# Kernel optimization log

Hardware: AMD Instinct MI355X
Metric: run time of the kernel (lower is better)

Reference implementation:

```python
import jax, jax.numpy as jnp
import numpy as np

B, S, D = 2, 2048, 4096
H, KV, HD = 32, 8, 128
THETA = 10000.0


def rotate_half(x):
    x1, x2 = x[..., : HD // 2], x[..., HD // 2 :]
    return jnp.concatenate((-x2, x1), axis=-1)


def setup_inputs() -> dict:
    key = jax.random.key(0)
    ks = jax.random.split(key, 8)
    s = 1.0 / np.sqrt(D)
    return {
        "hidden_states": jax.random.normal(ks[0], (B, S, D), jnp.float32),
        "modality_indicators": jax.random.randint(ks[1], (B, S), 0, 2, jnp.int64 if jax.config.jax_enable_x64 else jnp.int32),
        "position_ids": jnp.arange(S, dtype=jnp.int32),
        "Wq": jax.random.normal(ks[2], (D, H * HD), jnp.float32) * s,
        "Wk0": jax.random.normal(ks[3], (D, KV * HD), jnp.float32) * s,
        "Wk1": jax.random.normal(ks[4], (D, KV * HD), jnp.float32) * s,
        "Wv0": jax.random.normal(ks[5], (D, KV * HD), jnp.float32) * s,
        "Wv1": jax.random.normal(ks[6], (D, KV * HD), jnp.float32) * s,
        "Wo": jax.random.normal(ks[7], (H * HD, D), jnp.float32) * s,
    }


def reference(hidden_states, modality_indicators, position_ids, Wq, Wk0, Wk1, Wv0, Wv1, Wo):
    x = hidden_states
    # Multiway (modality-routed) k/v projections: per-token select between two linears.
    sel = (modality_indicators == 1)[..., None]  # [B,S,1]
    q = x @ Wq                                   # [B,S,H*HD]
    k = jnp.where(sel, x @ Wk1, x @ Wk0)         # [B,S,KV*HD]
    v = jnp.where(sel, x @ Wv1, x @ Wv0)

    q = q.reshape(B, S, H, HD).transpose(0, 2, 1, 3)    # [B,H,S,HD]
    k = k.reshape(B, S, KV, HD).transpose(0, 2, 1, 3)   # [B,KV,S,HD]
    v = v.reshape(B, S, KV, HD).transpose(0, 2, 1, 3)

    # RoPE cache and application (emb = cat(freqs, freqs))
    inv_freq = 1.0 / (THETA ** (jnp.arange(0, HD, 2, dtype=jnp.float32) / HD))
    freqs = position_ids.astype(jnp.float32)[:, None] * inv_freq[None, :]   # [S,HD/2]
    emb = jnp.concatenate((freqs, freqs), axis=-1)                          # [S,HD]
    cos = jnp.cos(emb)[None, None, :, :]                                    # [1,1,S,HD]
    sin = jnp.sin(emb)[None, None, :, :]
    q = q * cos + rotate_half(q) * sin
    k = k * cos + rotate_half(k) * sin

    # GQA: repeat kv heads
    n_rep = H // KV
    k = jnp.repeat(k, n_rep, axis=1)  # [B,H,S,HD]
    v = jnp.repeat(v, n_rep, axis=1)

    scores = jnp.einsum("bhqd,bhkd->bhqk", q, k) / np.sqrt(HD)
    causal = jnp.tril(jnp.ones((S, S), dtype=bool))
    scores = jnp.where(causal[None, None], scores, jnp.finfo(scores.dtype).min)
    attn = jax.nn.softmax(scores, axis=-1)
    ctx = jnp.einsum("bhqk,bhkd->bhqd", attn, v)            # [B,H,S,HD]
    ctx = ctx.transpose(0, 2, 1, 3).reshape(B, S, H * HD)
    return ctx @ Wo
```

## Files before the change

kernel.cpp:

```cpp
#include <hip/hip_runtime.h>

typedef unsigned short u16;
typedef unsigned int   u32;
using bf16x8 = __attribute__((ext_vector_type(8))) __bf16;
using f32x4  = __attribute__((ext_vector_type(4))) float;
using f32x16 = __attribute__((ext_vector_type(16))) float;
using u32x4  = __attribute__((ext_vector_type(4))) unsigned int;
using ushort8 = __attribute__((ext_vector_type(8))) unsigned short;


__device__ __forceinline__ u16 f2bf(float f) {
  u32 u = __builtin_bit_cast(u32, f);
  return (u16)((u + 0x7fffu + ((u >> 16) & 1u)) >> 16);
}
__device__ __forceinline__ float bf2f(u16 h) {
  return __builtin_bit_cast(float, (u32)h << 16);
}
__device__ __forceinline__ f32x4 mfma16(bf16x8 a, bf16x8 b, f32x4 c) {
  return __builtin_amdgcn_mfma_f32_16x16x32_bf16(a, b, c, 0, 0, 0);
}
__device__ __forceinline__ f32x16 mfma32(bf16x8 a, bf16x8 b, f32x16 c) {
  return __builtin_amdgcn_mfma_f32_32x32x16_bf16(a, b, c, 0, 0, 0);
}
__device__ __forceinline__ f32x16 zero16() {
  f32x16 z;
#pragma unroll
  for (int i = 0; i < 16; ++i) z[i] = 0.f;
  return z;
}
__device__ __forceinline__ void g2l16(const void* gp, void* lp) {
  __builtin_amdgcn_global_load_lds(
      (__attribute__((address_space(1))) void*)(void*)gp,
      (__attribute__((address_space(3))) void*)lp, 16, 0, 0);
}

__global__ void k_cvt(const float* __restrict__ in, u16* __restrict__ out, int n4) {
  int i = blockIdx.x * 256 + threadIdx.x;
  if (i >= n4) return;
  float4 v = ((const float4*)in)[i];
  ushort4 o;
  o.x = f2bf(v.x); o.y = f2bf(v.y); o.z = f2bf(v.z); o.w = f2bf(v.w);
  ((ushort4*)out)[i] = o;
}

__global__ __launch_bounds__(256) void k_tcvt(const float* __restrict__ in, u16* __restrict__ out,
                                              int K, int N) {
  __shared__ u16 t[64][72];
  const int n0 = blockIdx.x * 64, k0 = blockIdx.y * 64;
  const int tid = threadIdx.x;
  const int r = tid >> 2, c4 = (tid & 3) * 16;
  const float* src = in + (size_t)(k0 + r) * N + n0 + c4;
#pragma unroll
  for (int q = 0; q < 4; ++q) {
    float4 v = *(const float4*)(src + 4 * q);
    t[c4 + 4 * q + 0][r] = f2bf(v.x);
    t[c4 + 4 * q + 1][r] = f2bf(v.y);
    t[c4 + 4 * q + 2][r] = f2bf(v.z);
    t[c4 + 4 * q + 3][r] = f2bf(v.w);
  }
  __syncthreads();
  u16* dst = out + (size_t)(n0 + r) * K + k0 + c4;
#pragma unroll
  for (int hh = 0; hh < 2; ++hh)
    *(ushort8*)(dst + 8 * hh) = *(const ushort8*)(&t[r][c4 + 8 * hh]);
}

__global__ void k_scan(const int* __restrict__ mod, int* __restrict__ perm, int* __restrict__ meta) {
  __shared__ int ps[1024];
  const int b = blockIdx.x, t = threadIdx.x;
  perm[b * 2304 + t] = -1;
  perm[b * 2304 + 1024 + t] = -1;
  if (t < 256) perm[b * 2304 + 2048 + t] = -1;
  const int i0 = 2 * t, i1 = 2 * t + 1;
  const int f0 = (mod[b * 2048 + i0] != 1) ? 1 : 0;
  const int f1 = (mod[b * 2048 + i1] != 1) ? 1 : 0;
  const int sum = f0 + f1;
  ps[t] = sum;
  __syncthreads();
  for (int off = 1; off < 1024; off <<= 1) {
    int v = (t >= off) ? ps[t - off] : 0;
    __syncthreads();
    ps[t] += v;
    __syncthreads();
  }
  const int total0 = ps[1023];
  const int excl = ps[t] - sum;
  const int nt0 = (total0 + 255) >> 8;
  const int off1 = nt0 * 256;
  const int s0 = f0 ? excl : off1 + (i0 - excl);
  const int s1 = f1 ? (excl + f0) : off1 + (i1 - (excl + f0));
  perm[b * 2304 + s0] = i0;
  perm[b * 2304 + s1] = i1;
  if (t == 0) { meta[b * 2] = total0; meta[b * 2 + 1] = nt0; }
}

#define TILE_BODY(T, VMLIT, DOSTAGE)                                         \
  {                                                                          \
    asm volatile("s_waitcnt vmcnt(" VMLIT ")" ::: "memory");                 \
    __builtin_amdgcn_s_barrier();                                            \
    __builtin_amdgcn_sched_barrier(0);                                       \
    const u16* base_ = lds + ((T) & 3) * 16384;                              \
    bf16x8 bfr[4], afr[4];                                                   \
    _Pragma("unroll")                                                        \
    for (int nf = 0; nf < 4; ++nf)                                           \
      bfr[nf] = *(const bf16x8*)(base_ + boff + nf * 512);                   \
    _Pragma("unroll")                                                        \
    for (int mf = 0; mf < 4; ++mf)                                           \
      afr[mf] = *(const bf16x8*)(base_ + aoff + mf * 512);                   \
    if (DOSTAGE) stageA((T) + 3);                                            \
    asm volatile("s_waitcnt lgkmcnt(0)" ::: "memory");                       \
    __builtin_amdgcn_sched_barrier(0);                                       \
    __builtin_amdgcn_s_setprio(1);                                           \
    _Pragma("unroll")                                                        \
    for (int mf = 0; mf < 4; ++mf)                                           \
      _Pragma("unroll")                                                      \
      for (int nf = 0; nf < 4; ++nf)                                         \
        acc[mf][nf] = mfma16(afr[mf], bfr[nf], acc[mf][nf]);                 \
    __builtin_amdgcn_s_setprio(0);                                           \
    __builtin_amdgcn_s_barrier();                                            \
    _Pragma("unroll")                                                        \
    for (int mf = 0; mf < 4; ++mf)                                           \
      afr[mf] = *(const bf16x8*)(base_ + aoff + (mf + 4) * 512);             \
    if (DOSTAGE) stageB((T) + 3);                                            \
    asm volatile("s_waitcnt lgkmcnt(0)" ::: "memory");                       \
    __builtin_amdgcn_sched_barrier(0);                                       \
    __builtin_amdgcn_s_setprio(1);                                           \
    _Pragma("unroll")                                                        \
    for (int mf = 0; mf < 4; ++mf)                                           \
      _Pragma("unroll")                                                      \
      for (int nf = 0; nf < 4; ++nf)                                         \
        acc[mf + 4][nf] = mfma16(afr[mf], bfr[nf], acc[mf + 4][nf]);         \
    __builtin_amdgcn_s_setprio(0);                                           \
  }

#define GEMM_MAIN_LOOP()                                                     \
  stageA(0); stageB(0); stageA(1); stageB(1); stageA(2); stageB(2);          \
  for (int t = 0; t < 125; ++t) TILE_BODY(t, "8", true);                     \
  TILE_BODY(125, "8", false);                                                \
  TILE_BODY(126, "4", false);                                                \
  TILE_BODY(127, "0", false);

__global__ __launch_bounds__(512, 2) void k_gemm8(const u16* __restrict__ A, const u16* __restrict__ Bt,
                                                  float* __restrict__ Cp) {
  __shared__ u16 lds[4 * 16384];
  const int tid = threadIdx.x, wid = tid >> 6, l = tid & 63, g = l >> 4, li = l & 15;
  const int wr = wid >> 2, wc = wid & 3;
  const int bid = blockIdx.x;
  const int swz = (bid & 7) * 32 + (bid >> 3);
  const int m0 = (swz >> 4) * 256, n0 = (swz & 15) * 256;

  const int bo = wid * 2048 + l * 16;
  const int srow = bo >> 6;
  const int sgg = (l & 3) ^ ((l >> 3) & 3);
  const u16* pA0 = A + (size_t)(m0 + srow) * 4096 + sgg * 8;
  const u16* pA1 = pA0 + (size_t)16 * 4096;
  const u16* pB0 = Bt + (size_t)(n0 + srow) * 4096 + sgg * 8;
  const u16* pB1 = pB0 + (size_t)16 * 4096;

  auto stageA = [&](int t) {
    u16* da = (u16*)lds + (t & 3) * 16384 + wid * 1024;
    g2l16(pA0 + t * 32, da);
    g2l16(pA1 + t * 32, da + 512);
  };
  auto stageB = [&](int t) {
    u16* db = (u16*)lds + (t & 3) * 16384 + wid * 1024 + 8192;
    g2l16(pB0 + t * 32, db);
    g2l16(pB1 + t * 32, db + 512);
  };

  const int lsl8 = (g ^ ((li >> 1) & 3)) * 8;
  const int aoff = (wr * 128 + li) * 32 + lsl8;
  const int boff = 8192 + (wc * 64 + li) * 32 + lsl8;

  const f32x4 vzero = {0.f, 0.f, 0.f, 0.f};
  f32x4 acc[8][4];
#pragma unroll
  for (int m = 0; m < 8; ++m)
#pragma unroll
    for (int n = 0; n < 4; ++n) acc[m][n] = vzero;

  GEMM_MAIN_LOOP();

#pragma unroll
  for (int mf = 0; mf < 8; ++mf)
#pragma unroll
    for (int nf = 0; nf < 4; ++nf)
#pragma unroll
      for (int j = 0; j < 4; ++j) {
        int row = m0 + wr * 128 + mf * 16 + g * 4 + j;
        int col = n0 + wc * 64 + nf * 16 + li;
        Cp[(size_t)row * 4096 + col] = acc[mf][nf][j];
      }
}

__global__ __launch_bounds__(512, 2) void k_gemmQKV(const u16* __restrict__ Xb, const u16* __restrict__ WqT,
                                                    const u16* __restrict__ B0, const u16* __restrict__ B1,
                                                    const int* __restrict__ perm, const int* __restrict__ meta,
                                                    u16* __restrict__ Qr, u16* __restrict__ Ksel,
                                                    u16* __restrict__ Vsel) {
  __shared__ u16 lds[4 * 16384];
  const int tid = threadIdx.x, wid = tid >> 6, l = tid & 63, g = l >> 4, li = l & 15;
  const int wr = wid >> 2, wc = wid & 3;
  const int bid = blockIdx.x;
  const bool isQ = bid < 256;

  const int bo = wid * 2048 + l * 16;
  const int srow = bo >> 6;
  const int sgg = (l & 3) ^ ((l >> 3) & 3);

  int m0 = 0, n0 = 0, bb = 0, tm = 0;
  const u16 *pA0, *pA1, *pB0;
  if (isQ) {
    const int swz = (bid & 7) * 32 + (bid >> 3);
    m0 = (swz >> 4) * 256; n0 = (swz & 15) * 256;
    pA0 = Xb + (size_t)(m0 + srow) * 4096 + sgg * 8;
    pA1 = pA0 + (size_t)16 * 4096;
    pB0 = WqT + (size_t)(n0 + srow) * 4096 + sgg * 8;
  } else {
    const int kb = bid - 256;
    const int seg = kb >> 3;
    n0 = (kb & 7) * 256;
    bb = seg / 9; tm = seg % 9;
    const int nt0 = meta[bb * 2 + 1];
    const u16* Bt = (tm >= nt0) ? B1 : B0;
    int t0 = perm[bb * 2304 + tm * 256 + srow];
    int t1 = perm[bb * 2304 + tm * 256 + srow + 16];
    if (t0 < 0) t0 = 0;
    if (t1 < 0) t1 = 0;
    pA0 = Xb + ((size_t)bb * 2048 + t0) * 4096 + sgg * 8;
    pA1 = Xb + ((size_t)bb * 2048 + t1) * 4096 + sgg * 8;
    pB0 = Bt + (size_t)(n0 + srow) * 4096 + sgg * 8;
  }
  const u16* pB1 = pB0 + (size_t)16 * 4096;

  auto stageA = [&](int t) {
    u16* da = (u16*)lds + (t & 3) * 16384 + wid * 1024;
    g2l16(pA0 + t * 32, da);
    g2l16(pA1 + t * 32, da + 512);
  };
  auto stageB = [&](int t) {
    u16* db = (u16*)lds + (t & 3) * 16384 + wid * 1024 + 8192;
    g2l16(pB0 + t * 32, db);
    g2l16(pB1 + t * 32, db + 512);
  };

  const int lsl8 = (g ^ ((li >> 1) & 3)) * 8;
  const int aoff = (wr * 128 + li) * 32 + lsl8;
  const int boff = 8192 + (wc * 64 + li) * 32 + lsl8;

  const f32x4 vzero = {0.f, 0.f, 0.f, 0.f};
  f32x4 acc[8][4];
#pragma unroll
  for (int m = 0; m < 8; ++m)
#pragma unroll
    for (int n = 0; n < 4; ++n) acc[m][n] = vzero;

  GEMM_MAIN_LOOP();

  if (isQ) {
#pragma unroll
    for (int mf = 0; mf < 8; ++mf)
#pragma unroll
      for (int nf = 0; nf < 4; ++nf)
#pragma unroll
        for (int j = 0; j < 4; ++j) {
          int row = m0 + wr * 128 + mf * 16 + g * 4 + j;
          int col = n0 + wc * 64 + nf * 16 + li;
          int b = row >> 11, s = row & 2047, h = col >> 7, d = col & 127;
          Qr[(((size_t)(b * 32 + h)) * 2048 + s) * 128 + d] = f2bf(acc[mf][nf][j]);
        }
  } else {
#pragma unroll
    for (int mf = 0; mf < 8; ++mf)
#pragma unroll
      for (int nf = 0; nf < 4; ++nf)
#pragma unroll
        for (int j = 0; j < 4; ++j) {
          int slot = tm * 256 + wr * 128 + mf * 16 + g * 4 + j;
          int tok = perm[bb * 2304 + slot];
          if (tok >= 0) {
            int col = n0 + wc * 64 + nf * 16 + li;
            int kv = col >> 10, hh = (col >> 7) & 7, d = col & 127;
            u16* dst = (kv ? Vsel : Ksel) + (((size_t)(bb * 8 + hh)) * 2048 + tok) * 128 + d;
            *dst = f2bf(acc[mf][nf][j]);
          }
        }
  }
}

__global__ void k_ropeq(u16* __restrict__ Q, const int* __restrict__ pos) {
  int row = blockIdx.x * 4 + (threadIdx.x >> 6);
  int l = threadIdx.x & 63;
  int s = row & 2047;
  u16* p = Q + (size_t)row * 128;
  float x1 = bf2f(p[l]), x2 = bf2f(p[l + 64]);
  float ang = (float)pos[s] * expf((float)l * -0.14391156831212787f);
  float cs = cosf(ang), sn = sinf(ang);
  const float sc = 0.08838834764831845f;
  p[l] = f2bf((x1 * cs - x2 * sn) * sc);
  p[l + 64] = f2bf((x2 * cs + x1 * sn) * sc);
}

__global__ void k_kvprep(const u16* __restrict__ Ks, const u16* __restrict__ Vs,
                         const int* __restrict__ pos,
                         u16* __restrict__ Kr, u16* __restrict__ Vt) {
  __shared__ u16 Vl[64][136];
  int blk = blockIdx.x;
  int st = blk & 31, kvh = (blk >> 5) & 7, b = blk >> 8;
  int s0 = st * 64;
  int tid = threadIdx.x, wid = tid >> 6, l = tid & 63;
  float invf = expf((float)l * -0.14391156831212787f);
  size_t slab = (size_t)(b * 8 + kvh) * 2048;
  for (int rr = 0; rr < 16; ++rr) {
    int r = wid * 16 + rr;
    int s = s0 + r;
    const u16* ks = Ks + (slab + s) * 128;
    const u16* vs = Vs + (slab + s) * 128;
    float ang = (float)pos[s] * invf;
    float cs = cosf(ang), sn = sinf(ang);
    float x1 = bf2f(ks[l]), x2 = bf2f(ks[l + 64]);
    u16* kd = Kr + (slab + s) * 128;
    kd[l] = f2bf(x1 * cs - x2 * sn);
    kd[l + 64] = f2bf(x2 * cs + x1 * sn);
    Vl[r][l] = vs[l];
    Vl[r][l + 64] = vs[l + 64];
  }
  __syncthreads();
  int d = tid >> 1, si0 = (tid & 1) * 32;
  u16* vd = Vt + ((size_t)(b * 8 + kvh) * 128 + d) * 2048 + s0 + si0;
#pragma unroll
  for (int k4 = 0; k4 < 8; ++k4) {
    ushort4 o;
    o.x = Vl[si0 + k4 * 4 + 0][d];
    o.y = Vl[si0 + k4 * 4 + 1][d];
    o.z = Vl[si0 + k4 * 4 + 2][d];
    o.w = Vl[si0 + k4 * 4 + 3][d];
    *(ushort4*)(vd + k4 * 4) = o;
  }
}

__global__ __launch_bounds__(256, 2) void k_attn(const u16* __restrict__ Q, const u16* __restrict__ Kr,
                                                 const u16* __restrict__ Vt, u16* __restrict__ ctx) {
  __shared__ u16 Kl[2 * 64 * 128];
  __shared__ u16 Vl[2 * 128 * 64];
  const int bh = blockIdx.x;
  const int p = blockIdx.y;
  const int b = bh >> 5, h = bh & 31, kvh = h >> 2;
  const int tid = threadIdx.x, w = tid >> 6, l = tid & 63;
  const int lo5 = l & 31, hi = l >> 5;
  const bool hib = hi != 0;
  const size_t kvslab = (size_t)(b * 8 + kvh) * 2048;
  const u16* Kg = Kr + kvslab * 128;
  const u16* Vg = Vt + kvslab * 128;
  const float L2E = 1.4426950408889634f;

  auto stage = [&](int kt, int bi) {
#pragma unroll
    for (int i = 0; i < 4; ++i) {
      int c = w * 4 + i;
      int slot = c * 1024 + l * 16;
      {
        int row = slot >> 8;
        int inner = (slot & 255) ^ ((row & 15) << 4);
        g2l16((const char*)Kg + kt * 16384 + row * 256 + inner,
              (char*)Kl + bi * 16384 + c * 1024);
      }
      {
        int row = slot >> 7;
        int inner = (slot & 127) ^ ((row & 7) << 4);
        g2l16((const char*)Vg + (size_t)row * 4096 + kt * 128 + inner,
              (char*)Vl + bi * 16384 + c * 1024);
      }
    }
  };

  for (int hf = 0; hf < 2; ++hf) {
    const int qi = hf ? (15 - p) : p;
    const int q0 = qi * 128;
    const int qlane = q0 + w * 32 + lo5;
    const u16* qrow = Q + ((size_t)bh * 2048 + qlane) * 128;
    bf16x8 qf[8];
#pragma unroll
    for (int kk = 0; kk < 8; ++kk) qf[kk] = *(const bf16x8*)(qrow + kk * 16 + hi * 8);

    f32x16 ot[4];
#pragma unroll
    for (int i = 0; i < 4; ++i) ot[i] = zero16();
    float m = -1e30f, ls = 0.f;

    const int nkt = 2 * qi + 2;
    stage(0, 0);
    stage(1, 1);
    for (int kt = 0; kt < nkt; ++kt) {
      if (kt + 1 < nkt) {
        asm volatile("s_waitcnt vmcnt(8)" ::: "memory");
      } else {
        asm volatile("s_waitcnt vmcnt(0)" ::: "memory");
      }
      __builtin_amdgcn_s_barrier();
      __builtin_amdgcn_sched_barrier(0);
      const char* kbase = (const char*)Kl + (kt & 1) * 16384;
      const char* vbase = (const char*)Vl + (kt & 1) * 16384;
      const int ktb = kt * 64;
      if (ktb <= q0 + w * 32 + 31) {
        f32x16 st[2];
        st[0] = zero16(); st[1] = zero16();
#pragma unroll
        for (int kk = 0; kk < 8; ++kk) {
          bf16x8 kfr[2];
#pragma unroll
          for (int mf = 0; mf < 2; ++mf) {
            int row = mf * 32 + lo5;
            kfr[mf] = *(const bf16x8*)(kbase + row * 256 + ((kk * 32 + hi * 16) ^ ((row & 15) << 4)));
          }
          __builtin_amdgcn_s_setprio(1);
          st[0] = mfma32(kfr[0], qf[kk], st[0]);
          st[1] = mfma32(kfr[1], qf[kk], st[1]);
          __builtin_amdgcn_s_setprio(0);
        }
        if (ktb + 63 > q0 + w * 32) {
#pragma unroll
          for (int mf = 0; mf < 2; ++mf)
#pragma unroll
            for (int r = 0; r < 16; ++r) {
              int kg = ktb + mf * 32 + (r & 3) + 8 * (r >> 2) + 4 * hi;
              if (kg > qlane) st[mf][r] = -3.0e38f;
            }
        }
        float t[16];
#pragma unroll
        for (int r = 0; r < 16; ++r) t[r] = fmaxf(st[0][r], st[1][r]);
#pragma unroll
        for (int s = 8; s >= 1; s >>= 1)
#pragma unroll
          for (int r = 0; r < s; ++r) t[r] = fmaxf(t[r], t[r + s]);
        float pmax = fmaxf(t[0], __shfl_xor(t[0], 32));
        if (!__all(pmax <= m + 8.f)) {
          float nm = fmaxf(m, pmax);
          float resc = exp2f((m - nm) * L2E);
          m = nm;
          ls *= resc;
#pragma unroll
          for (int i = 0; i < 4; ++i)
#pragma unroll
            for (int r = 0; r < 16; ++r) ot[i][r] *= resc;
        }
#pragma unroll
        for (int mf = 0; mf < 2; ++mf)
#pragma unroll
          for (int r = 0; r < 16; ++r) st[mf][r] = exp2f((st[mf][r] - m) * L2E);
        float u[16];
#pragma unroll
        for (int r = 0; r < 16; ++r) u[r] = st[0][r] + st[1][r];
#pragma unroll
        for (int s = 8; s >= 1; s >>= 1)
#pragma unroll
          for (int r = 0; r < s; ++r) u[r] += u[r + s];
        ls += u[0] + __shfl_xor(u[0], 32);
        u32 pkv[16];
#pragma unroll
        for (int mf = 0; mf < 2; ++mf)
#pragma unroll
          for (int tt = 0; tt < 8; ++tt) {
            u32 r;
            asm("v_cvt_pk_bf16_f32 %0, %1, %2" : "=v"(r) : "v"(st[mf][2 * tt]), "v"(st[mf][2 * tt + 1]));
            pkv[mf * 8 + tt] = r;
          }
        bf16x8 pfrag[4];
#pragma unroll
        for (int kk = 0; kk < 4; ++kk) {
          int c = (kk >> 1) * 8 + (kk & 1) * 4;
          u32 m0 = hib ? pkv[c + 2] : pkv[c + 0];
          u32 m1 = hib ? pkv[c + 3] : pkv[c + 1];
          u32 s0 = hib ? pkv[c + 0] : pkv[c + 2];
          u32 s1 = hib ? pkv[c + 1] : pkv[c + 3];
          u32 r0 = (u32)__shfl_xor((int)s0, 32);
          u32 r1 = (u32)__shfl_xor((int)s1, 32);
          u32x4 wv = {hib ? r0 : m0, hib ? r1 : m1, hib ? m0 : r0, hib ? m1 : r1};
          pfrag[kk] = __builtin_bit_cast(bf16x8, wv);
        }
#pragma unroll
        for (int mfV = 0; mfV < 4; ++mfV) {
          int row = mfV * 32 + lo5;
          const char* vb = vbase + row * 128;
          int sw = (row & 7) << 4;
          bf16x8 vf[4];
#pragma unroll
          for (int kk = 0; kk < 4; ++kk)
            vf[kk] = *(const bf16x8*)(vb + ((kk * 32 + hi * 16) ^ sw));
          __builtin_amdgcn_s_setprio(1);
#pragma unroll
          for (int kk = 0; kk < 4; ++kk) ot[mfV] = mfma32(vf[kk], pfrag[kk], ot[mfV]);
          __builtin_amdgcn_s_setprio(0);
        }
      }
      __builtin_amdgcn_s_barrier();
      if (kt + 2 < nkt) stage(kt + 2, kt & 1);
    }
    float inv = 1.0f / ls;
    u16* crow = ctx + ((size_t)(b * 2048) + qlane) * 4096 + h * 128;
#pragma unroll
    for (int mfV = 0; mfV < 4; ++mfV)
#pragma unroll
      for (int rq = 0; rq < 4; ++rq) {
        ushort4 o4;
        o4.x = f2bf(ot[mfV][rq * 4 + 0] * inv);
        o4.y = f2bf(ot[mfV][rq * 4 + 1] * inv);
        o4.z = f2bf(ot[mfV][rq * 4 + 2] * inv);
        o4.w = f2bf(ot[mfV][rq * 4 + 3] * inv);
        *(ushort4*)(crow + mfV * 32 + rq * 8 + hi * 4) = o4;
      }
  }
}

extern "C" void kernel_launch(void* const* d_in, const int* in_sizes, int n_in,
                              void* d_out, int out_size, void* d_ws, size_t ws_size,
                              hipStream_t stream) {
  (void)in_sizes; (void)n_in; (void)out_size; (void)ws_size;
  const float* X   = (const float*)d_in[0];
  const int*   mod = (const int*)d_in[1];
  const int*   pos = (const int*)d_in[2];
  const float* Wq  = (const float*)d_in[3];
  const float* Wk0 = (const float*)d_in[4];
  const float* Wk1 = (const float*)d_in[5];
  const float* Wv0 = (const float*)d_in[6];
  const float* Wv1 = (const float*)d_in[7];
  const float* Wo  = (const float*)d_in[8];
  float* out = (float*)d_out;

  u16* p = (u16*)d_ws;
  auto take = [&](size_t n) { u16* r = p; p += n; return r; };
  u16* Xb    = take(16777216);
  u16* WqT   = take(16777216);
  u16* WoT   = take(16777216);
  u16* Wkv0T = take(8388608);
  u16* Wkv1T = take(8388608);
  u16* Qr    = take(16777216);
  u16* Ksel  = take(4194304);
  u16* Vsel  = take(4194304);
  int* perm  = (int*)take(9216);
  int* meta  = (int*)take(64);
  u16* Kr  = WqT;
  u16* Vtr = WqT + 4194304;
  u16* ctx = Xb;

  k_cvt<<<dim3(16384), 256, 0, stream>>>(X, Xb, 4194304);
  k_scan<<<dim3(2), 1024, 0, stream>>>(mod, perm, meta);
  k_tcvt<<<dim3(64, 64), 256, 0, stream>>>(Wq, WqT, 4096, 4096);
  k_tcvt<<<dim3(16, 64), 256, 0, stream>>>(Wk0, Wkv0T,                4096, 1024);
  k_tcvt<<<dim3(16, 64), 256, 0, stream>>>(Wv0, Wkv0T + 1024 * 4096,  4096, 1024);
  k_tcvt<<<dim3(16, 64), 256, 0, stream>>>(Wk1, Wkv1T,                4096, 1024);
  k_tcvt<<<dim3(16, 64), 256, 0, stream>>>(Wv1, Wkv1T + 1024 * 4096,  4096, 1024);
  k_tcvt<<<dim3(64, 64), 256, 0, stream>>>(Wo, WoT, 4096, 4096);

  k_gemmQKV<<<dim3(400), 512, 0, stream>>>(Xb, WqT, Wkv0T, Wkv1T, perm, meta, Qr, Ksel, Vsel);

  k_ropeq<<<dim3(32768), 256, 0, stream>>>(Qr, pos);
  k_kvprep<<<dim3(512), 256, 0, stream>>>(Ksel, Vsel, pos, Kr, Vtr);

  k_attn<<<dim3(64, 8), 256, 0, stream>>>(Qr, Kr, Vtr, ctx);

  k_gemm8<<<dim3(256), 512, 0, stream>>>(ctx, WoT, out);
}
```

Baseline: 566.2 us.

## Use 16-wave GEMM blocks with single-barrier tiles and fuse prep kernel launches

Both GEMM kernels move from 512 to 1024 threads. Each wave now computes a 64x64 sub-tile instead of 128x64, stages one A and one B chunk per tile, and each K-step has one barrier instead of two, with the manual LDS waits dropped. Separately, the four K/V weight transposes are merged with the Wq transpose into one launch, and the Q RoPE and K/V RoPE-plus-V-transpose kernels are merged into one launch. The Wo transpose is moved after attention. The intent is to raise MFMA occupancy and latency hiding and to cut launch overhead. The risks are extra register pressure from the (1024,4) launch bound, which asks for more resident waves than a CU supports, and looser scheduling control without the sched barriers.

```diff
diff --git a/kernel.cpp b/kernel.cpp
--- a/kernel.cpp
+++ b/kernel.cpp
@@ -43,10 +43,9 @@
   ((ushort4*)out)[i] = o;
 }
 
-__global__ __launch_bounds__(256) void k_tcvt(const float* __restrict__ in, u16* __restrict__ out,
-                                              int K, int N) {
-  __shared__ u16 t[64][72];
-  const int n0 = blockIdx.x * 64, k0 = blockIdx.y * 64;
+__device__ __forceinline__ void tcvt_tile(const float* __restrict__ in, u16* __restrict__ out,
+                                          int K, int N, int nt, int kt, u16 (*t)[72]) {
+  const int n0 = nt * 64, k0 = kt * 64;
   const int tid = threadIdx.x;
   const int r = tid >> 2, c4 = (tid & 3) * 16;
   const float* src = in + (size_t)(k0 + r) * N + n0 + c4;
@@ -63,6 +62,30 @@
 #pragma unroll
   for (int hh = 0; hh < 2; ++hh)
     *(ushort8*)(dst + 8 * hh) = *(const ushort8*)(&t[r][c4 + 8 * hh]);
+}
+
+__global__ __launch_bounds__(256) void k_tcvt(const float* __restrict__ in, u16* __restrict__ out,
+                                              int K, int N) {
+  __shared__ u16 t[64][72];
+  tcvt_tile(in, out, K, N, blockIdx.x, blockIdx.y, t);
+}
+
+__global__ __launch_bounds__(256) void k_tcvt5(const float* __restrict__ Wq, const float* __restrict__ Wk0,
+                                               const float* __restrict__ Wv0, const float* __restrict__ Wk1,
+                                               const float* __restrict__ Wv1, u16* __restrict__ WqT,
+                                               u16* __restrict__ Wkv0T, u16* __restrict__ Wkv1T) {
+  __shared__ u16 t[64][72];
+  int bid = blockIdx.x;
+  if (bid < 4096) {
+    tcvt_tile(Wq, WqT, 4096, 4096, bid & 63, bid >> 6, t);
+  } else {
+    int r = bid - 4096;
+    int mat = r >> 10, rr = r & 1023;
+    const float* src = (mat == 0) ? Wk0 : (mat == 1) ? Wv0 : (mat == 2) ? Wk1 : Wv1;
+    u16* dst = (mat == 0) ? Wkv0T : (mat == 1) ? (Wkv0T + (size_t)1024 * 4096)
+                                  : (mat == 2) ? Wkv1T : (Wkv1T + (size_t)1024 * 4096);
+    tcvt_tile(src, dst, 4096, 1024, rr & 15, rr >> 4, t);
+  }
 }
 
 __global__ void k_scan(const int* __restrict__ mod, int* __restrict__ perm, int* __restrict__ meta) {
@@ -107,9 +130,7 @@
     _Pragma("unroll")                                                        \
     for (int mf = 0; mf < 4; ++mf)                                           \
       afr[mf] = *(const bf16x8*)(base_ + aoff + mf * 512);                   \
-    if (DOSTAGE) stageA((T) + 3);                                            \
-    asm volatile("s_waitcnt lgkmcnt(0)" ::: "memory");                       \
-    __builtin_amdgcn_sched_barrier(0);                                       \
+    if (DOSTAGE) stage((T) + 3);                                             \
     __builtin_amdgcn_s_setprio(1);                                           \
     _Pragma("unroll")                                                        \
     for (int mf = 0; mf < 4; ++mf)                                           \
@@ -117,31 +138,17 @@
       for (int nf = 0; nf < 4; ++nf)                                         \
         acc[mf][nf] = mfma16(afr[mf], bfr[nf], acc[mf][nf]);                 \
     __builtin_amdgcn_s_setprio(0);                                           \
-    __builtin_amdgcn_s_barrier();                                            \
-    _Pragma("unroll")                                                        \
-    for (int mf = 0; mf < 4; ++mf)                                           \
-      afr[mf] = *(const bf16x8*)(base_ + aoff + (mf + 4) * 512);             \
-    if (DOSTAGE) stageB((T) + 3);                                            \
-    asm volatile("s_waitcnt lgkmcnt(0)" ::: "memory");                       \
-    __builtin_amdgcn_sched_barrier(0);                                       \
-    __builtin_amdgcn_s_setprio(1);                                           \
-    _Pragma("unroll")                                                        \
-    for (int mf = 0; mf < 4; ++mf)                                           \
-      _Pragma("unroll")                                                      \
-      for (int nf = 0; nf < 4; ++nf)                                         \
-        acc[mf + 4][nf] = mfma16(afr[mf], bfr[nf], acc[mf + 4][nf]);         \
-    __builtin_amdgcn_s_setprio(0);                                           \
   }
 
 #define GEMM_MAIN_LOOP()                                                     \
-  stageA(0); stageB(0); stageA(1); stageB(1); stageA(2); stageB(2);          \
-  for (int t = 0; t < 125; ++t) TILE_BODY(t, "8", true);                     \
-  TILE_BODY(125, "8", false);                                                \
-  TILE_BODY(126, "4", false);                                                \
+  stage(0); stage(1); stage(2);                                              \
+  for (int t = 0; t < 125; ++t) TILE_BODY(t, "4", true);                     \
+  TILE_BODY(125, "4", false);                                                \
+  TILE_BODY(126, "2", false);                                                \
   TILE_BODY(127, "0", false);
 
-__global__ __launch_bounds__(512, 2) void k_gemm8(const u16* __restrict__ A, const u16* __restrict__ Bt,
-                                                  float* __restrict__ Cp) {
+__global__ __launch_bounds__(1024, 4) void k_gemm8(const u16* __restrict__ A, const u16* __restrict__ Bt,
+                                                   float* __restrict__ Cp) {
   __shared__ u16 lds[4 * 16384];
   const int tid = threadIdx.x, wid = tid >> 6, l = tid & 63, g = l >> 4, li = l & 15;
   const int wr = wid >> 2, wc = wid & 3;
@@ -149,73 +156,63 @@
   const int swz = (bid & 7) * 32 + (bid >> 3);
   const int m0 = (swz >> 4) * 256, n0 = (swz & 15) * 256;
 
-  const int bo = wid * 2048 + l * 16;
-  const int srow = bo >> 6;
+  const int srow = wid * 16 + (l >> 2);
   const int sgg = (l & 3) ^ ((l >> 3) & 3);
-  const u16* pA0 = A + (size_t)(m0 + srow) * 4096 + sgg * 8;
-  const u16* pA1 = pA0 + (size_t)16 * 4096;
-  const u16* pB0 = Bt + (size_t)(n0 + srow) * 4096 + sgg * 8;
-  const u16* pB1 = pB0 + (size_t)16 * 4096;
-
-  auto stageA = [&](int t) {
-    u16* da = (u16*)lds + (t & 3) * 16384 + wid * 1024;
-    g2l16(pA0 + t * 32, da);
-    g2l16(pA1 + t * 32, da + 512);
+  const u16* pA = A + (size_t)(m0 + srow) * 4096 + sgg * 8;
+  const u16* pB = Bt + (size_t)(n0 + srow) * 4096 + sgg * 8;
+
+  auto stage = [&](int t) {
+    u16* da = (u16*)lds + (t & 3) * 16384 + wid * 512;
+    g2l16(pA + t * 32, da);
+    g2l16(pB + t * 32, da + 8192);
   };
-  auto stageB = [&](int t) {
-    u16* db = (u16*)lds + (t & 3) * 16384 + wid * 1024 + 8192;
-    g2l16(pB0 + t * 32, db);
-    g2l16(pB1 + t * 32, db + 512);
-  };
 
   const int lsl8 = (g ^ ((li >> 1) & 3)) * 8;
-  const int aoff = (wr * 128 + li) * 32 + lsl8;
+  const int aoff = (wr * 64 + li) * 32 + lsl8;
   const int boff = 8192 + (wc * 64 + li) * 32 + lsl8;
 
   const f32x4 vzero = {0.f, 0.f, 0.f, 0.f};
-  f32x4 acc[8][4];
-#pragma unroll
-  for (int m = 0; m < 8; ++m)
+  f32x4 acc[4][4];
+#pragma unroll
+  for (int m = 0; m < 4; ++m)
 #pragma unroll
     for (int n = 0; n < 4; ++n) acc[m][n] = vzero;
 
   GEMM_MAIN_LOOP();
 
 #pragma unroll
-  for (int mf = 0; mf < 8; ++mf)
+  for (int mf = 0; mf < 4; ++mf)
 #pragma unroll
     for (int nf = 0; nf < 4; ++nf)
 #pragma unroll
       for (int j = 0; j < 4; ++j) {
-        int row = m0 + wr * 128 + mf * 16 + g * 4 + j;
+        int row = m0 + wr * 64 + mf * 16 + g * 4 + j;
         int col = n0 + wc * 64 + nf * 16 + li;
         Cp[(size_t)row * 4096 + col] = acc[mf][nf][j];
       }
 }
 
-__global__ __launch_bounds__(512, 2) void k_gemmQKV(const u16* __restrict__ Xb, const u16* __restrict__ WqT,
-                                                    const u16* __restrict__ B0, const u16* __restrict__ B1,
-                                                    const int* __restrict__ perm, const int* __restrict__ meta,
-                                                    u16* __restrict__ Qr, u16* __restrict__ Ksel,
-                                                    u16* __restrict__ Vsel) {
+__global__ __launch_bounds__(1024, 4) void k_gemmQKV(const u16* __restrict__ Xb, const u16* __restrict__ WqT,
+                                                     const u16* __restrict__ B0, const u16* __restrict__ B1,
+                                                     const int* __restrict__ perm, const int* __restrict__ meta,
+                                                     u16* __restrict__ Qr, u16* __restrict__ Ksel,
+                                                     u16* __restrict__ Vsel) {
   __shared__ u16 lds[4 * 16384];
   const int tid = threadIdx.x, wid = tid >> 6, l = tid & 63, g = l >> 4, li = l & 15;
   const int wr = wid >> 2, wc = wid & 3;
   const int bid = blockIdx.x;
   const bool isQ = bid < 256;
 
-  const int bo = wid * 2048 + l * 16;
-  const int srow = bo >> 6;
+  const int srow = wid * 16 + (l >> 2);
   const int sgg = (l & 3) ^ ((l >> 3) & 3);
 
   int m0 = 0, n0 = 0, bb = 0, tm = 0;
-  const u16 *pA0, *pA1, *pB0;
+  const u16 *pA, *pB;
   if (isQ) {
     const int swz = (bid & 7) * 32 + (bid >> 3);
     m0 = (swz >> 4) * 256; n0 = (swz & 15) * 256;
-    pA0 = Xb + (size_t)(m0 + srow) * 4096 + sgg * 8;
-    pA1 = pA0 + (size_t)16 * 4096;
-    pB0 = WqT + (size_t)(n0 + srow) * 4096 + sgg * 8;
+    pA = Xb + (size_t)(m0 + srow) * 4096 + sgg * 8;
+    pB = WqT + (size_t)(n0 + srow) * 4096 + sgg * 8;
   } else {
     const int kb = bid - 256;
     const int seg = kb >> 3;
@@ -224,34 +221,25 @@
     const int nt0 = meta[bb * 2 + 1];
     const u16* Bt = (tm >= nt0) ? B1 : B0;
     int t0 = perm[bb * 2304 + tm * 256 + srow];
-    int t1 = perm[bb * 2304 + tm * 256 + srow + 16];
     if (t0 < 0) t0 = 0;
-    if (t1 < 0) t1 = 0;
-    pA0 = Xb + ((size_t)bb * 2048 + t0) * 4096 + sgg * 8;
-    pA1 = Xb + ((size_t)bb * 2048 + t1) * 4096 + sgg * 8;
-    pB0 = Bt + (size_t)(n0 + srow) * 4096 + sgg * 8;
-  }
-  const u16* pB1 = pB0 + (size_t)16 * 4096;
-
-  auto stageA = [&](int t) {
-    u16* da = (u16*)lds + (t & 3) * 16384 + wid * 1024;
-    g2l16(pA0 + t * 32, da);
-    g2l16(pA1 + t * 32, da + 512);
+    pA = Xb + ((size_t)bb * 2048 + t0) * 4096 + sgg * 8;
+    pB = Bt + (size_t)(n0 + srow) * 4096 + sgg * 8;
+  }
+
+  auto stage = [&](int t) {
+    u16* da = (u16*)lds + (t & 3) * 16384 + wid * 512;
+    g2l16(pA + t * 32, da);
+    g2l16(pB + t * 32, da + 8192);
   };
-  auto stageB = [&](int t) {
-    u16* db = (u16*)lds + (t & 3) * 16384 + wid * 1024 + 8192;
-    g2l16(pB0 + t * 32, db);
-    g2l16(pB1 + t * 32, db + 512);
-  };
 
   const int lsl8 = (g ^ ((li >> 1) & 3)) * 8;
-  const int aoff = (wr * 128 + li) * 32 + lsl8;
+  const int aoff = (wr * 64 + li) * 32 + lsl8;
   const int boff = 8192 + (wc * 64 + li) * 32 + lsl8;
 
   const f32x4 vzero = {0.f, 0.f, 0.f, 0.f};
-  f32x4 acc[8][4];
-#pragma unroll
-  for (int m = 0; m < 8; ++m)
+  f32x4 acc[4][4];
+#pragma unroll
+  for (int m = 0; m < 4; ++m)
 #pragma unroll
     for (int n = 0; n < 4; ++n) acc[m][n] = vzero;
 
@@ -259,24 +247,24 @@
 
   if (isQ) {
 #pragma unroll
-    for (int mf = 0; mf < 8; ++mf)
+    for (int mf = 0; mf < 4; ++mf)
 #pragma unroll
       for (int nf = 0; nf < 4; ++nf)
 #pragma unroll
         for (int j = 0; j < 4; ++j) {
-          int row = m0 + wr * 128 + mf * 16 + g * 4 + j;
+          int row = m0 + wr * 64 + mf * 16 + g * 4 + j;
           int col = n0 + wc * 64 + nf * 16 + li;
           int b = row >> 11, s = row & 2047, h = col >> 7, d = col & 127;
           Qr[(((size_t)(b * 32 + h)) * 2048 + s) * 128 + d] = f2bf(acc[mf][nf][j]);
         }
   } else {
 #pragma unroll
-    for (int mf = 0; mf < 8; ++mf)
+    for (int mf = 0; mf < 4; ++mf)
 #pragma unroll
       for (int nf = 0; nf < 4; ++nf)
 #pragma unroll
         for (int j = 0; j < 4; ++j) {
-          int slot = tm * 256 + wr * 128 + mf * 16 + g * 4 + j;
+          int slot = tm * 256 + wr * 64 + mf * 16 + g * 4 + j;
           int tok = perm[bb * 2304 + slot];
           if (tok >= 0) {
             int col = n0 + wc * 64 + nf * 16 + li;
@@ -288,54 +276,55 @@
   }
 }
 
-__global__ void k_ropeq(u16* __restrict__ Q, const int* __restrict__ pos) {
-  int row = blockIdx.x * 4 + (threadIdx.x >> 6);
-  int l = threadIdx.x & 63;
-  int s = row & 2047;
-  u16* p = Q + (size_t)row * 128;
-  float x1 = bf2f(p[l]), x2 = bf2f(p[l + 64]);
-  float ang = (float)pos[s] * expf((float)l * -0.14391156831212787f);
-  float cs = cosf(ang), sn = sinf(ang);
-  const float sc = 0.08838834764831845f;
-  p[l] = f2bf((x1 * cs - x2 * sn) * sc);
-  p[l + 64] = f2bf((x2 * cs + x1 * sn) * sc);
-}
-
-__global__ void k_kvprep(const u16* __restrict__ Ks, const u16* __restrict__ Vs,
-                         const int* __restrict__ pos,
-                         u16* __restrict__ Kr, u16* __restrict__ Vt) {
+__global__ __launch_bounds__(256) void k_ropekv(u16* __restrict__ Q, const u16* __restrict__ Ks,
+                                                const u16* __restrict__ Vs, const int* __restrict__ pos,
+                                                u16* __restrict__ Kr, u16* __restrict__ Vt) {
   __shared__ u16 Vl[64][136];
-  int blk = blockIdx.x;
-  int st = blk & 31, kvh = (blk >> 5) & 7, b = blk >> 8;
-  int s0 = st * 64;
-  int tid = threadIdx.x, wid = tid >> 6, l = tid & 63;
-  float invf = expf((float)l * -0.14391156831212787f);
-  size_t slab = (size_t)(b * 8 + kvh) * 2048;
-  for (int rr = 0; rr < 16; ++rr) {
-    int r = wid * 16 + rr;
-    int s = s0 + r;
-    const u16* ks = Ks + (slab + s) * 128;
-    const u16* vs = Vs + (slab + s) * 128;
+  const int bid = blockIdx.x;
+  const int tid = threadIdx.x, l = tid & 63;
+  const float invf = expf((float)l * -0.14391156831212787f);
+  if (bid < 32768) {
+    int row = bid * 4 + (tid >> 6);
+    int s = row & 2047;
+    u16* p = Q + (size_t)row * 128;
+    float x1 = bf2f(p[l]), x2 = bf2f(p[l + 64]);
     float ang = (float)pos[s] * invf;
     float cs = cosf(ang), sn = sinf(ang);
-    float x1 = bf2f(ks[l]), x2 = bf2f(ks[l + 64]);
-    u16* kd = Kr + (slab + s) * 128;
-    kd[l] = f2bf(x1 * cs - x2 * sn);
-    kd[l + 64] = f2bf(x2 * cs + x1 * sn);
-    Vl[r][l] = vs[l];
-    Vl[r][l + 64] = vs[l + 64];
-  }
-  __syncthreads();
-  int d = tid >> 1, si0 = (tid & 1) * 32;
-  u16* vd = Vt + ((size_t)(b * 8 + kvh) * 128 + d) * 2048 + s0 + si0;
-#pragma unroll
-  for (int k4 = 0; k4 < 8; ++k4) {
-    ushort4 o;
-    o.x = Vl[si0 + k4 * 4 + 0][d];
-    o.y = Vl[si0 + k4 * 4 + 1][d];
-    o.z = Vl[si0 + k4 * 4 + 2][d];
-    o.w = Vl[si0 + k4 * 4 + 3][d];
-    *(ushort4*)(vd + k4 * 4) = o;
+    const float sc = 0.08838834764831845f;
+    p[l] = f2bf((x1 * cs - x2 * sn) * sc);
+    p[l + 64] = f2bf((x2 * cs + x1 * sn) * sc);
+  } else {
+    int blk = bid - 32768;
+    int st = blk & 31, kvh = (blk >> 5) & 7, b = blk >> 8;
+    int s0 = st * 64;
+    int wid = tid >> 6;
+    size_t slab = (size_t)(b * 8 + kvh) * 2048;
+    for (int rr = 0; rr < 16; ++rr) {
+      int r = wid * 16 + rr;
+      int s = s0 + r;
+      const u16* ks = Ks + (slab + s) * 128;
+      const u16* vs = Vs + (slab + s) * 128;
+      float ang = (float)pos[s] * invf;
+      float cs = cosf(ang), sn = sinf(ang);
+      float x1 = bf2f(ks[l]), x2 = bf2f(ks[l + 64]);
+      u16* kd = Kr + (slab + s) * 128;
+      kd[l] = f2bf(x1 * cs - x2 * sn);
+      kd[l + 64] = f2bf(x2 * cs + x1 * sn);
+      Vl[r][l] = vs[l];
+      Vl[r][l + 64] = vs[l + 64];
+    }
+    __syncthreads();
+    int d = tid >> 1, si0 = (tid & 1) * 32;
+    u16* vd = Vt + ((size_t)(b * 8 + kvh) * 128 + d) * 2048 + s0 + si0;
+#pragma unroll
+    for (int k4 = 0; k4 < 8; ++k4) {
+      ushort4 o;
+      o.x = Vl[si0 + k4 * 4 + 0][d];
+      o.y = Vl[si0 + k4 * 4 + 1][d];
+      o.z = Vl[si0 + k4 * 4 + 2][d];
+      o.w = Vl[si0 + k4 * 4 + 3][d];
+      *(ushort4*)(vd + k4 * 4) = o;
+    }
   }
 }
 
@@ -546,19 +535,15 @@
 
   k_cvt<<<dim3(16384), 256, 0, stream>>>(X, Xb, 4194304);
   k_scan<<<dim3(2), 1024, 0, stream>>>(mod, perm, meta);
-  k_tcvt<<<dim3(64, 64), 256, 0, stream>>>(Wq, WqT, 4096, 4096);
-  k_tcvt<<<dim3(16, 64), 256, 0, stream>>>(Wk0, Wkv0T,                4096, 1024);
-  k_tcvt<<<dim3(16, 64), 256, 0, stream>>>(Wv0, Wkv0T + 1024 * 4096,  4096, 1024);
-  k_tcvt<<<dim3(16, 64), 256, 0, stream>>>(Wk1, Wkv1T,                4096, 1024);
-  k_tcvt<<<dim3(16, 64), 256, 0, stream>>>(Wv1, Wkv1T + 1024 * 4096,  4096, 1024);
+  k_tcvt5<<<dim3(8192), 256, 0, stream>>>(Wq, Wk0, Wv0, Wk1, Wv1, WqT, Wkv0T, Wkv1T);
+
+  k_gemmQKV<<<dim3(400), 1024, 0, stream>>>(Xb, WqT, Wkv0T, Wkv1T, perm, meta, Qr, Ksel, Vsel);
+
+  k_ropekv<<<dim3(33280), 256, 0, stream>>>(Qr, Ksel, Vsel, pos, Kr, Vtr);
+
+  k_attn<<<dim3(64, 8), 256, 0, stream>>>(Qr, Kr, Vtr, ctx);
+
   k_tcvt<<<dim3(64, 64), 256, 0, stream>>>(Wo, WoT, 4096, 4096);
 
-  k_gemmQKV<<<dim3(400), 512, 0, stream>>>(Xb, WqT, Wkv0T, Wkv1T, perm, meta, Qr, Ksel, Vsel);
-
-  k_ropeq<<<dim3(32768), 256, 0, stream>>>(Qr, pos);
-  k_kvprep<<<dim3(512), 256, 0, stream>>>(Ksel, Vsel, pos, Kr, Vtr);
-
-  k_attn<<<dim3(64, 8), 256, 0, stream>>>(Qr, Kr, Vtr, ctx);
-
-  k_gemm8<<<dim3(256), 512, 0, stream>>>(ctx, WoT, out);
-}
+  k_gemm8<<<dim3(256), 1024, 0, stream>>>(ctx, WoT, out);
+}
```

Result: faster. 550.7 us (-2.7%).
